# Kernel optimization log

Hardware: AMD Instinct MI355X
Metric: run time of the kernel (lower is better)

Reference implementation:

```python
import jax, jax.numpy as jnp
import numpy as np

B, IN, H, M, N, SR = 64, 256, 512, 64, 8192, 3


def setup_inputs() -> dict:
    key = jax.random.key(0)
    ks = jax.random.split(key, 20)
    u = lambda k, sh, b: jax.random.uniform(k, sh, jnp.float32, -b, b)
    b_in = float(np.sqrt(6.0 / (IN + M + H)))
    b_k = float(np.sqrt(6.0 / (H + M)))
    b_c = float(np.sqrt(6.0 / (H + 3)))
    b_s = float(np.sqrt(6.0 / (H + SR)))
    b_w = float(np.sqrt(6.0 / (H + M)))
    # orthogonal-column recurrent weight, like the svd-U init in reset_weights
    rng = np.random.RandomState(0)
    W_hh = np.linalg.qr(rng.normal(0.0, 1.0, (4 * H, H)))[0].astype(np.float32)
    b_ih = jnp.zeros((4 * H,), jnp.float32).at[H:2 * H].set(1.0)  # forget-gate bias = 1
    return {
        'inp': jax.random.normal(ks[0], (B, IN), jnp.float32),
        'h': 0.1 * jax.random.normal(ks[1], (B, H), jnp.float32),
        'c': 0.1 * jax.random.normal(ks[2], (B, H), jnp.float32),
        'read_head': jax.random.uniform(ks[3], (B, N), jnp.float32) / N,
        'write_head': jax.random.uniform(ks[4], (B, N), jnp.float32) / N,
        'memory': 0.1 * jax.random.normal(ks[5], (B, N, M), jnp.float32),
        'W_ih': u(ks[6], (4 * H, IN + M), b_in),
        'b_ih': b_ih,
        'W_hh': jnp.asarray(W_hh),
        'b_hh': jnp.zeros((4 * H,), jnp.float32),
        'rk_w': u(ks[7], (M, H), b_k), 'rk_b': u(ks[8], (M,), b_k),
        'rc_w': u(ks[9], (3, H), b_c), 'rc_b': jnp.zeros((3,), jnp.float32),
        'rs_w': u(ks[10], (SR, H), b_s), 'rs_b': jnp.zeros((SR,), jnp.float32),
        'wk_w': u(ks[11], (M, H), b_k), 'wk_b': u(ks[12], (M,), b_k),
        'wc_w': u(ks[13], (3, H), b_c), 'wc_b': jnp.zeros((3,), jnp.float32),
        'ws_w': u(ks[14], (SR, H), b_s), 'ws_b': jnp.zeros((SR,), jnp.float32),
        'w_w': u(ks[15], (2 * M, H), b_w), 'w_b': jnp.zeros((2 * M,), jnp.float32),
    }


def _controller(hst, kw, kb, cw, cb, sw, sb):
    k = jnp.tanh(hst @ kw.T + kb)                       # [B, M]
    cv = hst @ cw.T + cb                                # [B, 3]
    s = jax.nn.softmax(hst @ sw.T + sb, axis=1)         # [B, SR]
    beta = jax.nn.relu(cv[:, 0:1]) + 1e-4
    g = jax.nn.sigmoid(cv[:, 1:2])
    gamma = jax.nn.relu(cv[:, 2:3]) + 1.0001
    return k, s, beta, g, gamma


def _get_address(Mem, head_tm1, k, s, beta, g, gamma):
    dot = jnp.einsum('bm,bnm->bn', k, Mem)              # [B, N]
    nM = jnp.sum(Mem * Mem, axis=2)                     # [B, N] (squared norms, as in source)
    nk = jnp.sum(k * k, axis=1, keepdims=True)          # [B, 1]
    content = jax.nn.softmax(beta * dot / (nM * nk), axis=1)
    inter = content * g + (1.0 - g) * head_tm1          # [B, N]
    inter_exp = jnp.concatenate([inter[:, -(SR - 1):], inter], axis=1)  # [B, N+SR-1]
    # circular-shift cross-correlation (per-sample conv1d in source), unrolled over SR taps
    out = sum(inter_exp[:, t:t + N] * s[:, t:t + 1] for t in range(SR))
    out = out ** gamma
    return out / jnp.sum(out, axis=1, keepdims=True)


def reference(inp, h, c, read_head, write_head, memory, W_ih, b_ih, W_hh, b_hh,
              rk_w, rk_b, rc_w, rc_b, rs_w, rs_b, wk_w, wk_b, wc_w, wc_b,
              ws_w, ws_b, w_w, w_b):
    # read addressing
    rk, rs, rbeta, rg, rgamma = _controller(h, rk_w, rk_b, rc_w, rc_b, rs_w, rs_b)
    r_head = _get_address(memory, read_head, rk, rs, rbeta, rg, rgamma)
    M_read = jnp.einsum('bn,bnm->bm', r_head, memory)   # [B, M]
    # LSTMCell controller (torch gate order i, f, g, o)
    x = jnp.concatenate([inp, M_read], axis=1)
    gates = x @ W_ih.T + b_ih + h @ W_hh.T + b_hh
    i_g, f_g, g_g, o_g = jnp.split(gates, 4, axis=1)
    c_new = jax.nn.sigmoid(f_g) * c + jax.nn.sigmoid(i_g) * jnp.tanh(g_g)
    h_new = jax.nn.sigmoid(o_g) * jnp.tanh(c_new)
    # write addressing + memory update
    wk, ws, wbeta, wg, wgamma = _controller(h_new, wk_w, wk_b, wc_w, wc_b, ws_w, ws_b)
    w_head = _get_address(memory, write_head, wk, ws, wbeta, wg, wgamma)
    write_all = h_new @ w_w.T + w_b
    e = jax.nn.sigmoid(write_all[:, :M])                # erase [B, M]
    a = write_all[:, M:]                                # add   [B, M]
    w = w_head[:, :, None]                              # [B, N, 1]
    M_out = memory * (1.0 - w * e[:, None, :]) + w * a[:, None, :]
    return (h_new, c_new, r_head, w_head, M_out)
```

## Files before the change

kernel.cpp:

```cpp
#include <hip/hip_runtime.h>
#include <hip/hip_bf16.h>
#include <math.h>

#define B_ 64
#define IN_ 256
#define H_ 512
#define M_ 64
#define N_ 8192
#define G4_ 2048

#define OFF_SCORE  0
#define OFF_GATES  524288
#define OFF_RK     655360
#define OFF_WK     659456
#define OFF_WA     663552
#define OFF_MREAD  671744
#define OFF_RBETA  675840
#define OFF_RG     675904
#define OFF_RGAMMA 675968
#define OFF_RNK    676032
#define OFF_RS     676096
#define OFF_WBETA  676352
#define OFF_WG     676416
#define OFF_WGAMMA 676480
#define OFF_WNK    676544
#define OFF_WS     676608

__device__ __forceinline__ float sigf(float x) { return 1.0f / (1.0f + expf(-x)); }

__global__ __launch_bounds__(256) void controller_kernel(
    const float* __restrict__ hsrc,
    const float* __restrict__ kw, const float* __restrict__ kb,
    const float* __restrict__ cw, const float* __restrict__ cb,
    const float* __restrict__ sw, const float* __restrict__ sb,
    const float* __restrict__ ww, const float* __restrict__ wb,
    float* __restrict__ k_out, float* __restrict__ beta_o,
    float* __restrict__ g_o, float* __restrict__ gamma_o,
    float* __restrict__ nk_o, float* __restrict__ s_o,
    float* __restrict__ wa_o)
{
    int b = blockIdx.x;
    __shared__ float hs[H_];
    __shared__ float tmp[6];
    __shared__ float kvals[M_];
    for (int i = threadIdx.x; i < H_; i += 256) hs[i] = hsrc[b * H_ + i];
    __syncthreads();
    int nout = wa_o ? 198 : 70;
    for (int o = threadIdx.x; o < nout; o += 256) {
        const float* wrow; float bias;
        if (o < 64)      { wrow = kw + o * H_;        bias = kb[o]; }
        else if (o < 67) { wrow = cw + (o - 64) * H_; bias = cb[o - 64]; }
        else if (o < 70) { wrow = sw + (o - 67) * H_; bias = sb[o - 67]; }
        else             { wrow = ww + (o - 70) * H_; bias = wb[o - 70]; }
        float acc = bias;
        #pragma unroll 4
        for (int k = 0; k < H_; ++k) acc += hs[k] * wrow[k];
        if (o < 64) {
            float kv = tanhf(acc);
            kvals[o] = kv;
            k_out[b * M_ + o] = kv;
        } else if (o < 70) {
            tmp[o - 64] = acc;
        } else {
            int j = o - 70;
            wa_o[b * 128 + j] = (j < 64) ? sigf(acc) : acc;
        }
    }
    __syncthreads();
    if (threadIdx.x == 0) {
        beta_o[b]  = fmaxf(tmp[0], 0.0f) + 1e-4f;
        g_o[b]     = sigf(tmp[1]);
        gamma_o[b] = fmaxf(tmp[2], 0.0f) + 1.0001f;
        float s0 = tmp[3], s1 = tmp[4], s2 = tmp[5];
        float mx = fmaxf(s0, fmaxf(s1, s2));
        float e0 = expf(s0 - mx), e1 = expf(s1 - mx), e2 = expf(s2 - mx);
        float ss = e0 + e1 + e2;
        s_o[b * 3 + 0] = e0 / ss; s_o[b * 3 + 1] = e1 / ss; s_o[b * 3 + 2] = e2 / ss;
        float nk = 0.0f;
        for (int m = 0; m < M_; ++m) nk += kvals[m] * kvals[m];
        nk_o[b] = nk;
    }
}

__global__ __launch_bounds__(256) void score_kernel(
    const float* __restrict__ mem, const float* __restrict__ kvec,
    const float* __restrict__ beta, const float* __restrict__ nk,
    float* __restrict__ score)
{
    int b = blockIdx.y;
    int lane = threadIdx.x & 63, wave = threadIdx.x >> 6;
    int mq = lane & 15, sub = lane >> 4;
    float4 k4 = ((const float4*)(kvec + b * M_))[mq];
    float be = beta[b], nkk = nk[b];
    const int chunk = N_ / 32;
    int base = blockIdx.x * chunk;
    const float4* memb = (const float4*)(mem + (size_t)b * N_ * M_);
    for (int it = 0; it < chunk / 16; ++it) {
        int n = base + it * 16 + wave * 4 + sub;
        float4 v = memb[(size_t)n * 16 + mq];
        float d  = v.x * k4.x + v.y * k4.y + v.z * k4.z + v.w * k4.w;
        float nm = v.x * v.x + v.y * v.y + v.z * v.z + v.w * v.w;
        #pragma unroll
        for (int off = 1; off < 16; off <<= 1) {
            d  += __shfl_xor(d, off);
            nm += __shfl_xor(nm, off);
        }
        if (mq == 0) score[(size_t)b * N_ + n] = be * d / (nm * nkk);
    }
}

__global__ __launch_bounds__(1024) void address_kernel(
    const float* __restrict__ score, const float* __restrict__ head_tm1,
    const float* __restrict__ g_, const float* __restrict__ gamma_,
    const float* __restrict__ s_, float* __restrict__ head_out)
{
    int b = blockIdx.x;
    __shared__ float inter[N_];
    __shared__ float red[16];
    int tid = threadIdx.x;
    const float* sc = score + (size_t)b * N_;

    float v[8];
    float mx = -1e30f;
    #pragma unroll
    for (int r = 0; r < 8; ++r) { v[r] = sc[tid + r * 1024]; mx = fmaxf(mx, v[r]); }
    #pragma unroll
    for (int off = 32; off; off >>= 1) mx = fmaxf(mx, __shfl_xor(mx, off));
    if ((tid & 63) == 0) red[tid >> 6] = mx;
    __syncthreads();
    mx = red[0];
    for (int i = 1; i < 16; ++i) mx = fmaxf(mx, red[i]);
    __syncthreads();

    float sum = 0.0f;
    #pragma unroll
    for (int r = 0; r < 8; ++r) { v[r] = expf(v[r] - mx); sum += v[r]; }
    #pragma unroll
    for (int off = 32; off; off >>= 1) sum += __shfl_xor(sum, off);
    if ((tid & 63) == 0) red[tid >> 6] = sum;
    __syncthreads();
    sum = 0.0f;
    for (int i = 0; i < 16; ++i) sum += red[i];
    float inv = 1.0f / sum;
    __syncthreads();

    float gb = g_[b], gm = gamma_[b];
    float s0 = s_[b * 3], s1 = s_[b * 3 + 1], s2 = s_[b * 3 + 2];
    const float* ht = head_tm1 + (size_t)b * N_;
    #pragma unroll
    for (int r = 0; r < 8; ++r) {
        int n = tid + r * 1024;
        inter[n] = gb * (v[r] * inv) + (1.0f - gb) * ht[n];
    }
    __syncthreads();

    float outv[8];
    float psum = 0.0f;
    #pragma unroll
    for (int r = 0; r < 8; ++r) {
        int n = tid + r * 1024;
        float o = s0 * inter[(n + N_ - 2) & (N_ - 1)]
                + s1 * inter[(n + N_ - 1) & (N_ - 1)]
                + s2 * inter[n];
        o = powf(fmaxf(o, 0.0f), gm);
        outv[r] = o;
        psum += o;
    }
    #pragma unroll
    for (int off = 32; off; off >>= 1) psum += __shfl_xor(psum, off);
    if ((tid & 63) == 0) red[tid >> 6] = psum;
    __syncthreads();
    psum = 0.0f;
    for (int i = 0; i < 16; ++i) psum += red[i];
    float inv2 = 1.0f / psum;
    float* ho = head_out + (size_t)b * N_;
    #pragma unroll
    for (int r = 0; r < 8; ++r) ho[tid + r * 1024] = outv[r] * inv2;
}

__global__ __launch_bounds__(256) void mread_kernel(
    const float* __restrict__ mem, const float* __restrict__ rhead,
    float* __restrict__ mread)
{
    int b = blockIdx.y;
    int lane = threadIdx.x & 63, wave = threadIdx.x >> 6;
    int mq = lane & 15, sub = lane >> 4;
    const int chunk = N_ / 32;
    int base = blockIdx.x * chunk;
    const float4* memb = (const float4*)(mem + (size_t)b * N_ * M_);
    const float* rh = rhead + (size_t)b * N_;
    float4 acc = make_float4(0.f, 0.f, 0.f, 0.f);
    for (int it = 0; it < chunk / 16; ++it) {
        int n = base + it * 16 + wave * 4 + sub;
        float w = rh[n];
        float4 v = memb[(size_t)n * 16 + mq];
        acc.x += w * v.x; acc.y += w * v.y; acc.z += w * v.z; acc.w += w * v.w;
    }
    #pragma unroll
    for (int off = 16; off < 64; off <<= 1) {
        acc.x += __shfl_xor(acc.x, off); acc.y += __shfl_xor(acc.y, off);
        acc.z += __shfl_xor(acc.z, off); acc.w += __shfl_xor(acc.w, off);
    }
    __shared__ float4 wsum[4][16];
    if (sub == 0) wsum[wave][mq] = acc;
    __syncthreads();
    if (threadIdx.x < 16) {
        float4 t = wsum[0][threadIdx.x];
        for (int w2 = 1; w2 < 4; ++w2) {
            float4 u = wsum[w2][threadIdx.x];
            t.x += u.x; t.y += u.y; t.z += u.z; t.w += u.w;
        }
        float* dst = mread + b * M_ + threadIdx.x * 4;
        atomicAdd(dst + 0, t.x); atomicAdd(dst + 1, t.y);
        atomicAdd(dst + 2, t.z); atomicAdd(dst + 3, t.w);
    }
}

__global__ __launch_bounds__(256) void gates_kernel(
    const float* __restrict__ inp, const float* __restrict__ mread,
    const float* __restrict__ h, const float* __restrict__ Wih,
    const float* __restrict__ bih, const float* __restrict__ Whh,
    const float* __restrict__ bhh, float* __restrict__ gates)
{
    int jb = blockIdx.x * 32;
    int tid = threadIdx.x;
    int bb = tid & 63;
    int jg = tid >> 6;
    __shared__ float Xs[64][65];
    __shared__ float Ws[32][65];
    float acc[8] = {0.f, 0.f, 0.f, 0.f, 0.f, 0.f, 0.f, 0.f};

    for (int kb = 0; kb < 320; kb += 64) {
        for (int i = tid; i < 64 * 64; i += 256) {
            int bl = i >> 6, kk = i & 63, k = kb + kk;
            Xs[bl][kk] = (k < IN_) ? inp[bl * IN_ + k] : mread[bl * M_ + (k - IN_)];
        }
        for (int i = tid; i < 32 * 64; i += 256) {
            int jj = i >> 6, kk = i & 63;
            Ws[jj][kk] = Wih[(size_t)(jb + jj) * 320 + kb + kk];
        }
        __syncthreads();
        for (int kk = 0; kk < 64; ++kk) {
            float xv = Xs[bb][kk];
            #pragma unroll
            for (int u = 0; u < 8; ++u) acc[u] += xv * Ws[jg * 8 + u][kk];
        }
        __syncthreads();
    }
    for (int kb = 0; kb < 512; kb += 64) {
        for (int i = tid; i < 64 * 64; i += 256) {
            int bl = i >> 6, kk = i & 63;
            Xs[bl][kk] = h[bl * H_ + kb + kk];
        }
        for (int i = tid; i < 32 * 64; i += 256) {
            int jj = i >> 6, kk = i & 63;
            Ws[jj][kk] = Whh[(size_t)(jb + jj) * 512 + kb + kk];
        }
        __syncthreads();
        for (int kk = 0; kk < 64; ++kk) {
            float xv = Xs[bb][kk];
            #pragma unroll
            for (int u = 0; u < 8; ++u) acc[u] += xv * Ws[jg * 8 + u][kk];
        }
        __syncthreads();
    }
    #pragma unroll
    for (int u = 0; u < 8; ++u) {
        int j = jb + jg * 8 + u;
        gates[bb * G4_ + j] = acc[u] + bih[j] + bhh[j];
    }
}

__global__ __launch_bounds__(256) void lstm_kernel(
    const float* __restrict__ gates, const float* __restrict__ c_in,
    float* __restrict__ h_new, float* __restrict__ c_new)
{
    int i = blockIdx.x * 256 + threadIdx.x;
    if (i >= B_ * H_) return;
    int b = i >> 9, hh = i & 511;
    const float* gb = gates + b * G4_;
    float ig = gb[hh], fg = gb[H_ + hh], gg = gb[2 * H_ + hh], og = gb[3 * H_ + hh];
    float cn = sigf(fg) * c_in[i] + sigf(ig) * tanhf(gg);
    float hn = sigf(og) * tanhf(cn);
    c_new[i] = cn;
    h_new[i] = hn;
}

__global__ __launch_bounds__(256) void writemem_kernel(
    const float* __restrict__ mem, const float* __restrict__ whead,
    const float* __restrict__ wa, float* __restrict__ mout)
{
    size_t i4 = (size_t)blockIdx.x * 256 + threadIdx.x;
    int mq = (int)(i4 & 15);
    int n  = (int)((i4 >> 4) & (N_ - 1));
    int b  = (int)(i4 >> 17);
    float w = whead[(size_t)b * N_ + n];
    float4 e4 = ((const float4*)(wa + b * 128))[mq];
    float4 a4 = ((const float4*)(wa + b * 128 + 64))[mq];
    float4 v = ((const float4*)mem)[i4];
    float4 o;
    o.x = v.x * (1.0f - w * e4.x) + w * a4.x;
    o.y = v.y * (1.0f - w * e4.y) + w * a4.y;
    o.z = v.z * (1.0f - w * e4.z) + w * a4.z;
    o.w = v.w * (1.0f - w * e4.w) + w * a4.w;
    ((float4*)mout)[i4] = o;
}

extern "C" void kernel_launch(void* const* d_in, const int* in_sizes, int n_in,
                              void* d_out, int out_size, void* d_ws, size_t ws_size,
                              hipStream_t stream) {
    (void)in_sizes; (void)n_in; (void)out_size; (void)ws_size;
    const float* inp     = (const float*)d_in[0];
    const float* h       = (const float*)d_in[1];
    const float* c       = (const float*)d_in[2];
    const float* rhead0  = (const float*)d_in[3];
    const float* whead0  = (const float*)d_in[4];
    const float* mem     = (const float*)d_in[5];
    const float* W_ih    = (const float*)d_in[6];
    const float* b_ih    = (const float*)d_in[7];
    const float* W_hh    = (const float*)d_in[8];
    const float* b_hh    = (const float*)d_in[9];
    const float* rk_w    = (const float*)d_in[10];
    const float* rk_b    = (const float*)d_in[11];
    const float* rc_w    = (const float*)d_in[12];
    const float* rc_b    = (const float*)d_in[13];
    const float* rs_w    = (const float*)d_in[14];
    const float* rs_b    = (const float*)d_in[15];
    const float* wk_w    = (const float*)d_in[16];
    const float* wk_b    = (const float*)d_in[17];
    const float* wc_w    = (const float*)d_in[18];
    const float* wc_b    = (const float*)d_in[19];
    const float* ws_w    = (const float*)d_in[20];
    const float* ws_b    = (const float*)d_in[21];
    const float* w_w     = (const float*)d_in[22];
    const float* w_b     = (const float*)d_in[23];

    float* ws = (float*)d_ws;
    float* out = (float*)d_out;
    float* h_new  = out;
    float* c_new  = out + 32768;
    float* r_head = out + 65536;
    float* w_head = out + 65536 + 524288;
    float* m_out  = out + 65536 + 2 * 524288;

    hipMemsetAsync(ws + OFF_MREAD, 0, M_ * B_ * sizeof(float) / 64 * 64, stream);

    controller_kernel<<<B_, 256, 0, stream>>>(
        h, rk_w, rk_b, rc_w, rc_b, rs_w, rs_b, nullptr, nullptr,
        ws + OFF_RK, ws + OFF_RBETA, ws + OFF_RG, ws + OFF_RGAMMA,
        ws + OFF_RNK, ws + OFF_RS, nullptr);
    score_kernel<<<dim3(32, B_), 256, 0, stream>>>(
        mem, ws + OFF_RK, ws + OFF_RBETA, ws + OFF_RNK, ws + OFF_SCORE);
    address_kernel<<<B_, 1024, 0, stream>>>(
        ws + OFF_SCORE, rhead0, ws + OFF_RG, ws + OFF_RGAMMA, ws + OFF_RS, r_head);
    mread_kernel<<<dim3(32, B_), 256, 0, stream>>>(mem, r_head, ws + OFF_MREAD);

    gates_kernel<<<G4_ / 32, 256, 0, stream>>>(
        inp, ws + OFF_MREAD, h, W_ih, b_ih, W_hh, b_hh, ws + OFF_GATES);
    lstm_kernel<<<(B_ * H_ + 255) / 256, 256, 0, stream>>>(
        ws + OFF_GATES, c, h_new, c_new);

    controller_kernel<<<B_, 256, 0, stream>>>(
        h_new, wk_w, wk_b, wc_w, wc_b, ws_w, ws_b, w_w, w_b,
        ws + OFF_WK, ws + OFF_WBETA, ws + OFF_WG, ws + OFF_WGAMMA,
        ws + OFF_WNK, ws + OFF_WS, ws + OFF_WA);
    score_kernel<<<dim3(32, B_), 256, 0, stream>>>(
        mem, ws + OFF_WK, ws + OFF_WBETA, ws + OFF_WNK, ws + OFF_SCORE);
    address_kernel<<<B_, 1024, 0, stream>>>(
        ws + OFF_SCORE, whead0, ws + OFF_WG, ws + OFF_WGAMMA, ws + OFF_WS, w_head);
    writemem_kernel<<<(B_ * N_ * M_ / 4) / 256, 256, 0, stream>>>(
        mem, w_head, ws + OFF_WA, m_out);
}
```

Baseline: 531.3 us.

## Parallelize controller matvecs across waves and shrink gates tiles for more blocks

The controller kernel moves from one block per batch row, with one thread per output and a serial dot product, to one wavefront per output row. Each wave does a shuffle-reduced dot product, and the key norm is accumulated with atomics into a zeroed workspace. The shift softmax moves into the address kernel so the controller needs no block-level sync. The gates GEMM is fused into a single K loop over the concatenated inputs, with 8 outputs per block instead of 32, giving 256 blocks instead of 64 and float4 LDS reads. The trade-off is that each block reloads the full X tile, so X is re-read more times overall.

```diff
diff --git a/kernel.cpp b/kernel.cpp
--- a/kernel.cpp
+++ b/kernel.cpp
@@ -15,16 +15,17 @@
 #define OFF_WK     659456
 #define OFF_WA     663552
 #define OFF_MREAD  671744
-#define OFF_RBETA  675840
-#define OFF_RG     675904
-#define OFF_RGAMMA 675968
-#define OFF_RNK    676032
-#define OFF_RS     676096
+#define OFF_RNK    675840
+#define OFF_WNK    675904
+#define ZERO_FLTS  4224
+#define OFF_RBETA  675968
+#define OFF_RG     676032
+#define OFF_RGAMMA 676096
+#define OFF_RS     676160
 #define OFF_WBETA  676352
 #define OFF_WG     676416
 #define OFF_WGAMMA 676480
-#define OFF_WNK    676544
-#define OFF_WS     676608
+#define OFF_WS     676544
 
 __device__ __forceinline__ float sigf(float x) { return 1.0f / (1.0f + expf(-x)); }
 
@@ -36,49 +37,45 @@
     const float* __restrict__ ww, const float* __restrict__ wb,
     float* __restrict__ k_out, float* __restrict__ beta_o,
     float* __restrict__ g_o, float* __restrict__ gamma_o,
-    float* __restrict__ nk_o, float* __restrict__ s_o,
-    float* __restrict__ wa_o)
-{
-    int b = blockIdx.x;
-    __shared__ float hs[H_];
-    __shared__ float tmp[6];
-    __shared__ float kvals[M_];
-    for (int i = threadIdx.x; i < H_; i += 256) hs[i] = hsrc[b * H_ + i];
-    __syncthreads();
-    int nout = wa_o ? 198 : 70;
-    for (int o = threadIdx.x; o < nout; o += 256) {
-        const float* wrow; float bias;
-        if (o < 64)      { wrow = kw + o * H_;        bias = kb[o]; }
-        else if (o < 67) { wrow = cw + (o - 64) * H_; bias = cb[o - 64]; }
-        else if (o < 70) { wrow = sw + (o - 67) * H_; bias = sb[o - 67]; }
-        else             { wrow = ww + (o - 70) * H_; bias = wb[o - 70]; }
-        float acc = bias;
-        #pragma unroll 4
-        for (int k = 0; k < H_; ++k) acc += hs[k] * wrow[k];
+    float* __restrict__ nk_o, float* __restrict__ s_raw,
+    float* __restrict__ wa_o, int nout)
+{
+    int b = blockIdx.y;
+    int wave = threadIdx.x >> 6, lane = threadIdx.x & 63;
+    int o = blockIdx.x * 4 + wave;
+    if (o >= nout) return;
+    const float* wrow; float bias;
+    if (o < 64)      { wrow = kw + (size_t)o * H_;        bias = kb[o]; }
+    else if (o < 67) { wrow = cw + (size_t)(o - 64) * H_; bias = cb[o - 64]; }
+    else if (o < 70) { wrow = sw + (size_t)(o - 67) * H_; bias = sb[o - 67]; }
+    else             { wrow = ww + (size_t)(o - 70) * H_; bias = wb[o - 70]; }
+    const float* hb = hsrc + (size_t)b * H_;
+    float acc = 0.0f;
+    #pragma unroll
+    for (int i = 0; i < 8; ++i) {
+        int k = lane + i * 64;
+        acc += hb[k] * wrow[k];
+    }
+    #pragma unroll
+    for (int off = 32; off; off >>= 1) acc += __shfl_xor(acc, off);
+    acc += bias;
+    if (lane == 0) {
         if (o < 64) {
             float kv = tanhf(acc);
-            kvals[o] = kv;
             k_out[b * M_ + o] = kv;
+            atomicAdd(&nk_o[b], kv * kv);
+        } else if (o == 64) {
+            beta_o[b] = fmaxf(acc, 0.0f) + 1e-4f;
+        } else if (o == 65) {
+            g_o[b] = sigf(acc);
+        } else if (o == 66) {
+            gamma_o[b] = fmaxf(acc, 0.0f) + 1.0001f;
         } else if (o < 70) {
-            tmp[o - 64] = acc;
+            s_raw[b * 3 + (o - 67)] = acc;
         } else {
             int j = o - 70;
             wa_o[b * 128 + j] = (j < 64) ? sigf(acc) : acc;
         }
-    }
-    __syncthreads();
-    if (threadIdx.x == 0) {
-        beta_o[b]  = fmaxf(tmp[0], 0.0f) + 1e-4f;
-        g_o[b]     = sigf(tmp[1]);
-        gamma_o[b] = fmaxf(tmp[2], 0.0f) + 1.0001f;
-        float s0 = tmp[3], s1 = tmp[4], s2 = tmp[5];
-        float mx = fmaxf(s0, fmaxf(s1, s2));
-        float e0 = expf(s0 - mx), e1 = expf(s1 - mx), e2 = expf(s2 - mx);
-        float ss = e0 + e1 + e2;
-        s_o[b * 3 + 0] = e0 / ss; s_o[b * 3 + 1] = e1 / ss; s_o[b * 3 + 2] = e2 / ss;
-        float nk = 0.0f;
-        for (int m = 0; m < M_; ++m) nk += kvals[m] * kvals[m];
-        nk_o[b] = nk;
     }
 }
 
@@ -144,8 +141,13 @@
     float inv = 1.0f / sum;
     __syncthreads();
 
+    float r0 = s_[b * 3], r1 = s_[b * 3 + 1], r2 = s_[b * 3 + 2];
+    float mx3 = fmaxf(r0, fmaxf(r1, r2));
+    float e0 = expf(r0 - mx3), e1 = expf(r1 - mx3), e2 = expf(r2 - mx3);
+    float ss = e0 + e1 + e2;
+    float s0 = e0 / ss, s1 = e1 / ss, s2 = e2 / ss;
+
     float gb = g_[b], gm = gamma_[b];
-    float s0 = s_[b * 3], s1 = s_[b * 3 + 1], s2 = s_[b * 3 + 2];
     const float* ht = head_tm1 + (size_t)b * N_;
     #pragma unroll
     for (int r = 0; r < 8; ++r) {
@@ -222,53 +224,43 @@
     const float* __restrict__ bih, const float* __restrict__ Whh,
     const float* __restrict__ bhh, float* __restrict__ gates)
 {
-    int jb = blockIdx.x * 32;
+    int jb = blockIdx.x * 8;
     int tid = threadIdx.x;
     int bb = tid & 63;
     int jg = tid >> 6;
-    __shared__ float Xs[64][65];
-    __shared__ float Ws[32][65];
-    float acc[8] = {0.f, 0.f, 0.f, 0.f, 0.f, 0.f, 0.f, 0.f};
-
-    for (int kb = 0; kb < 320; kb += 64) {
-        for (int i = tid; i < 64 * 64; i += 256) {
+    int j0 = jb + jg * 2;
+    __shared__ float Xs[64][68];
+    __shared__ float Ws[8][68];
+    float acc0 = 0.f, acc1 = 0.f;
+
+    for (int kb = 0; kb < 832; kb += 64) {
+        for (int i = tid; i < 4096; i += 256) {
             int bl = i >> 6, kk = i & 63, k = kb + kk;
-            Xs[bl][kk] = (k < IN_) ? inp[bl * IN_ + k] : mread[bl * M_ + (k - IN_)];
-        }
-        for (int i = tid; i < 32 * 64; i += 256) {
-            int jj = i >> 6, kk = i & 63;
-            Ws[jj][kk] = Wih[(size_t)(jb + jj) * 320 + kb + kk];
+            float xv;
+            if (k < IN_)            xv = inp[bl * IN_ + k];
+            else if (k < IN_ + M_)  xv = mread[bl * M_ + (k - IN_)];
+            else                    xv = h[bl * H_ + (k - IN_ - M_)];
+            Xs[bl][kk] = xv;
+        }
+        for (int i = tid; i < 512; i += 256) {
+            int jr = i >> 6, kk = i & 63, k = kb + kk;
+            Ws[jr][kk] = (k < IN_ + M_)
+                       ? Wih[(size_t)(jb + jr) * (IN_ + M_) + k]
+                       : Whh[(size_t)(jb + jr) * H_ + (k - IN_ - M_)];
         }
         __syncthreads();
-        for (int kk = 0; kk < 64; ++kk) {
-            float xv = Xs[bb][kk];
-            #pragma unroll
-            for (int u = 0; u < 8; ++u) acc[u] += xv * Ws[jg * 8 + u][kk];
+        #pragma unroll
+        for (int kk = 0; kk < 64; kk += 4) {
+            float4 x4 = *(const float4*)&Xs[bb][kk];
+            float4 w0 = *(const float4*)&Ws[jg * 2 + 0][kk];
+            float4 w1 = *(const float4*)&Ws[jg * 2 + 1][kk];
+            acc0 += x4.x * w0.x + x4.y * w0.y + x4.z * w0.z + x4.w * w0.w;
+            acc1 += x4.x * w1.x + x4.y * w1.y + x4.z * w1.z + x4.w * w1.w;
         }
         __syncthreads();
     }
-    for (int kb = 0; kb < 512; kb += 64) {
-        for (int i = tid; i < 64 * 64; i += 256) {
-            int bl = i >> 6, kk = i & 63;
-            Xs[bl][kk] = h[bl * H_ + kb + kk];
-        }
-        for (int i = tid; i < 32 * 64; i += 256) {
-            int jj = i >> 6, kk = i & 63;
-            Ws[jj][kk] = Whh[(size_t)(jb + jj) * 512 + kb + kk];
-        }
-        __syncthreads();
-        for (int kk = 0; kk < 64; ++kk) {
-            float xv = Xs[bb][kk];
-            #pragma unroll
-            for (int u = 0; u < 8; ++u) acc[u] += xv * Ws[jg * 8 + u][kk];
-        }
-        __syncthreads();
-    }
-    #pragma unroll
-    for (int u = 0; u < 8; ++u) {
-        int j = jb + jg * 8 + u;
-        gates[bb * G4_ + j] = acc[u] + bih[j] + bhh[j];
-    }
+    gates[bb * G4_ + j0]     = acc0 + bih[j0]     + bhh[j0];
+    gates[bb * G4_ + j0 + 1] = acc1 + bih[j0 + 1] + bhh[j0 + 1];
 }
 
 __global__ __launch_bounds__(256) void lstm_kernel(
@@ -343,27 +335,27 @@
     float* w_head = out + 65536 + 524288;
     float* m_out  = out + 65536 + 2 * 524288;
 
-    hipMemsetAsync(ws + OFF_MREAD, 0, M_ * B_ * sizeof(float) / 64 * 64, stream);
-
-    controller_kernel<<<B_, 256, 0, stream>>>(
-        h, rk_w, rk_b, rc_w, rc_b, rs_w, rs_b, nullptr, nullptr,
+    hipMemsetAsync(ws + OFF_MREAD, 0, ZERO_FLTS * sizeof(float), stream);
+
+    controller_kernel<<<dim3(18, B_), 256, 0, stream>>>(
+        h, rk_w, rk_b, rc_w, rc_b, rs_w, rs_b, w_w, w_b,
         ws + OFF_RK, ws + OFF_RBETA, ws + OFF_RG, ws + OFF_RGAMMA,
-        ws + OFF_RNK, ws + OFF_RS, nullptr);
+        ws + OFF_RNK, ws + OFF_RS, nullptr, 70);
     score_kernel<<<dim3(32, B_), 256, 0, stream>>>(
         mem, ws + OFF_RK, ws + OFF_RBETA, ws + OFF_RNK, ws + OFF_SCORE);
     address_kernel<<<B_, 1024, 0, stream>>>(
         ws + OFF_SCORE, rhead0, ws + OFF_RG, ws + OFF_RGAMMA, ws + OFF_RS, r_head);
     mread_kernel<<<dim3(32, B_), 256, 0, stream>>>(mem, r_head, ws + OFF_MREAD);
 
-    gates_kernel<<<G4_ / 32, 256, 0, stream>>>(
+    gates_kernel<<<G4_ / 8, 256, 0, stream>>>(
         inp, ws + OFF_MREAD, h, W_ih, b_ih, W_hh, b_hh, ws + OFF_GATES);
     lstm_kernel<<<(B_ * H_ + 255) / 256, 256, 0, stream>>>(
         ws + OFF_GATES, c, h_new, c_new);
 
-    controller_kernel<<<B_, 256, 0, stream>>>(
+    controller_kernel<<<dim3(50, B_), 256, 0, stream>>>(
         h_new, wk_w, wk_b, wc_w, wc_b, ws_w, ws_b, w_w, w_b,
         ws + OFF_WK, ws + OFF_WBETA, ws + OFF_WG, ws + OFF_WGAMMA,
-        ws + OFF_WNK, ws + OFF_WS, ws + OFF_WA);
+        ws + OFF_WNK, ws + OFF_WS, ws + OFF_WA, 198);
     score_kernel<<<dim3(32, B_), 256, 0, stream>>>(
         mem, ws + OFF_WK, ws + OFF_WBETA, ws + OFF_WNK, ws + OFF_SCORE);
     address_kernel<<<B_, 1024, 0, stream>>>(
```

Result: faster. 504.7 us (-5.0%).
